# Kernel optimization log

Hardware: AMD Instinct MI355X
Metric: run time of the kernel (lower is better)

## Reference

```python
import jax, jax.numpy as jnp
import numpy as np

D_MODEL = 768
N_HEADS = 12
D_HEAD = 64
INIT_RANGE = 0.02
IGNORE = -100000.0


def setup_inputs() -> dict:
    key = jax.random.key(0)
    ks = jax.random.split(key, 5)
    x = jax.random.normal(ks[0], (2, 2048, D_MODEL), dtype=jnp.float32)
    W_Q = INIT_RANGE * jax.random.normal(ks[1], (N_HEADS, D_MODEL, D_HEAD), dtype=jnp.float32)
    W_K = INIT_RANGE * jax.random.normal(ks[2], (N_HEADS, D_MODEL, D_HEAD), dtype=jnp.float32)
    W_V = INIT_RANGE * jax.random.normal(ks[3], (N_HEADS, D_MODEL, D_HEAD), dtype=jnp.float32)
    W_O = INIT_RANGE * jax.random.normal(ks[4], (N_HEADS, D_HEAD, D_MODEL), dtype=jnp.float32)
    b_Q = jnp.zeros((N_HEADS, D_HEAD), dtype=jnp.float32)
    b_K = jnp.zeros((N_HEADS, D_HEAD), dtype=jnp.float32)
    b_V = jnp.zeros((N_HEADS, D_HEAD), dtype=jnp.float32)
    b_O = jnp.zeros((D_MODEL,), dtype=jnp.float32)
    return {"x": x, "W_Q": W_Q, "b_Q": b_Q, "W_K": W_K, "b_K": b_K,
            "W_V": W_V, "b_V": b_V, "W_O": W_O, "b_O": b_O}


def reference(x, W_Q, b_Q, W_K, b_K, W_V, b_V, W_O, b_O):
    # x: [b, s, m]; W_*: [h, m, d]
    Q = jnp.einsum('bsm,hmd->bshd', x, W_Q) + b_Q  # [b, s, h, d]
    K = jnp.einsum('bsm,hmd->bshd', x, W_K) + b_K
    V = jnp.einsum('bsm,hmd->bshd', x, W_V) + b_V
    scores = jnp.einsum('bqhd,bkhd->bhqk', Q, K) / jnp.sqrt(jnp.float32(D_HEAD))
    s = scores.shape[-1]
    causal = jnp.triu(jnp.ones((s, s), dtype=bool), k=1)  # True above diagonal
    scores = jnp.where(causal, jnp.float32(IGNORE), scores)
    pattern = jax.nn.softmax(scores, axis=-1)  # [b, h, q, k]
    Z = jnp.einsum('bhqk,bkhd->bqhd', pattern, V)
    out = jnp.einsum('bqhd,hdm->bqm', Z, W_O) + b_O
    return out
```

## Files before the change

kernel.cpp:

```cpp
#include <hip/hip_runtime.h>
#include <hip/hip_bf16.h>

#define BATCH 2
#define SLEN 2048
#define NH 12
#define DM 768
#define DH 64
#define ROWS (BATCH*SLEN)
#define NQKV (3*DM)
#define NCHUNK 40

typedef __attribute__((ext_vector_type(8))) short bf16x8;
typedef __attribute__((ext_vector_type(4))) float f32x4;
typedef __attribute__((ext_vector_type(16))) float f32x16;
typedef unsigned short u16;
typedef unsigned int u32;
typedef __attribute__((ext_vector_type(4))) unsigned short u16x4;
typedef __attribute__((ext_vector_type(8))) unsigned short u16x8;

__device__ __forceinline__ u16 f2b(float f) {
    unsigned int u = __builtin_bit_cast(unsigned int, f);
    unsigned int r = (u + 0x7FFFu + ((u >> 16) & 1u)) >> 16;
    return (u16)r;
}
__device__ __forceinline__ float b2f(u16 v) {
    unsigned int u = ((unsigned int)v) << 16;
    return __builtin_bit_cast(float, u);
}

__device__ __forceinline__ void gload16(const u16* g, u16* l) {
    __builtin_amdgcn_global_load_lds(
        (const __attribute__((address_space(1))) unsigned int*)g,
        (__attribute__((address_space(3))) unsigned int*)l,
        16, 0, 0);
}


__global__ __launch_bounds__(256) void pack_all(const float* __restrict__ x,
                                                const float* __restrict__ WQ, const float* __restrict__ WK,
                                                const float* __restrict__ WV, const float* __restrict__ WO,
                                                u16* __restrict__ xb, u16* __restrict__ wqkv,
                                                u16* __restrict__ wo) {
    __shared__ u16 L[64 * 72];
    int blk = blockIdx.x;
    int t = threadIdx.x;
    if (blk < 1536) {
        int i = blk * 256 + t;
        const float4* xv = (const float4*)x;
        float4 a = xv[i * 2], b = xv[i * 2 + 1];
        u16x8 o;
        o[0] = f2b(a.x); o[1] = f2b(a.y); o[2] = f2b(a.z); o[3] = f2b(a.w);
        o[4] = f2b(b.x); o[5] = f2b(b.y); o[6] = f2b(b.z); o[7] = f2b(b.w);
        *(u16x8*)(xb + (size_t)i * 8) = o;
    } else if (blk < 1968) {
        int idx = blk - 1536;
        int mt = idx % 12, h = (idx / 12) % 12, sel = idx / 144;
        const float* W = sel == 0 ? WQ : (sel == 1 ? WK : WV);
        const float* src = W + ((size_t)h * DM + mt * 64) * DH;
        for (int j = 0; j < 4; j++) {
            int i = t + 256 * j;
            int r = i >> 4, cf = i & 15;
            float4 v = ((const float4*)src)[i];
            u16x4 o; o[0] = f2b(v.x); o[1] = f2b(v.y); o[2] = f2b(v.z); o[3] = f2b(v.w);
            *(u16x4*)&L[r * 72 + cf * 4] = o;
        }
        __syncthreads();
        u16* orow = wqkv + ((size_t)(sel * DM + h * DH)) * DM + mt * 64;
        for (int j = 0; j < 16; j++) {
            int e = t + 256 * j;
            int d = e >> 6, mm = e & 63;
            orow[(size_t)d * DM + mm] = L[mm * 72 + d];
        }
    } else {
        int idx = blk - 1968;
        int bi = idx % 12, bj = idx / 12;
        for (int j = 0; j < 4; j++) {
            int i = t + 256 * j;
            int r = i >> 4, cf = i & 15;
            float4 v = ((const float4*)(WO + (size_t)(bi * 64 + r) * DM + bj * 64))[cf];
            u16x4 o; o[0] = f2b(v.x); o[1] = f2b(v.y); o[2] = f2b(v.z); o[3] = f2b(v.w);
            *(u16x4*)&L[r * 72 + cf * 4] = o;
        }
        __syncthreads();
        for (int j = 0; j < 16; j++) {
            int e = t + 256 * j;
            int c = e >> 6, r = e & 63;
            wo[(size_t)(bj * 64 + c) * DM + bi * 64 + r] = L[r * 72 + c];
        }
    }
}


__global__ __launch_bounds__(256) void gemm_qkv(const u16* __restrict__ A, const u16* __restrict__ Bt,
                                                const float* __restrict__ bQ, const float* __restrict__ bK,
                                                const float* __restrict__ bV,
                                                u16* __restrict__ Qb, u16* __restrict__ Kb, u16* __restrict__ Vb) {
    __shared__ u16 S[128 * 64 + 96 * 64];
    u16* Al = S;
    u16* Bl = S + 128 * 64;
    int t = threadIdx.x;
    int n0 = blockIdx.x * 96, m0 = blockIdx.y * 128;
    int lane = t & 63, w = t >> 6;
    int ln = lane & 15, qd = lane >> 4;
    int wr = (w & 1) * 64, wc = (w >> 1) * 48;
    int srow = lane >> 3, slot = lane & 7;
    f32x4 acc[4][3] = {};

    for (int kt = 0; kt < DM / 64; kt++) {
        __syncthreads();
        for (int j = 0; j < 4; j++) {
            int r = w * 32 + j * 8 + srow;
            int gc = slot ^ (r & 7);
            gload16(A + (size_t)(m0 + r) * DM + kt * 64 + gc * 8, &Al[(w * 32 + j * 8) * 64]);
        }
        for (int j = 0; j < 3; j++) {
            int r = w * 24 + j * 8 + srow;
            int gc = slot ^ (r & 7);
            gload16(Bt + (size_t)(n0 + r) * DM + kt * 64 + gc * 8, &Bl[(w * 24 + j * 8) * 64]);
        }
        __syncthreads();
        for (int ks = 0; ks < 2; ks++) {
            int sl = ((ks * 4 + qd) ^ (ln & 7)) * 8;
            bf16x8 af[4], bfr[3];
            for (int rt = 0; rt < 4; rt++)
                af[rt] = *(const bf16x8*)&Al[(wr + rt * 16 + ln) * 64 + sl];
            for (int ct = 0; ct < 3; ct++)
                bfr[ct] = *(const bf16x8*)&Bl[(wc + ct * 16 + ln) * 64 + sl];
            for (int rt = 0; rt < 4; rt++)
                for (int ct = 0; ct < 3; ct++)
                    acc[rt][ct] = __builtin_amdgcn_mfma_f32_16x16x32_bf16(af[rt], bfr[ct], acc[rt][ct], 0, 0, 0);
        }
    }
    int sel = n0 / DM;
    if (sel == 2) {
        __syncthreads();
        for (int ct = 0; ct < 3; ct++) {
            int c = wc + ct * 16 + ln;
            float bv = bV[n0 - 2 * DM + c];
            for (int rt = 0; rt < 4; rt++) {
                int s = wr + rt * 16 + qd * 4;
                for (int r = 0; r < 4; r++)
                    S[c * 136 + s + r] = f2b(acc[rt][ct][r] + bv);
            }
        }
        __syncthreads();
        int bb = m0 >> 11, ss0 = m0 & 2047;
        for (int it = 0; it < 6; it++) {
            int e = t + it * 256;
            int c = e >> 4, ck = e & 15;
            int gcol = n0 - 2 * DM + c;
            int hh = gcol >> 6, dd = gcol & 63;
            u16x8 v = *(const u16x8*)&S[c * 136 + ck * 8];
            *(u16x8*)&Vb[(((size_t)bb * NH + hh) * DH + dd) * SLEN + ss0 + ck * 8] = v;
        }
    } else {
        const float* bias = sel == 0 ? bQ : bK;
        u16* Out = sel == 0 ? Qb : Kb;
        const float qs = sel == 0 ? 0.125f * 1.44269504f : 1.0f;
        for (int ct = 0; ct < 3; ct++) {
            int col = n0 - sel * DM + wc + ct * 16 + ln;
            int hh = col >> 6, dd = col & 63;
            float bv = bias[col];
            for (int rt = 0; rt < 4; rt++) {
                int row = m0 + wr + rt * 16 + qd * 4;
                for (int r = 0; r < 4; r++) {
                    int rg = row + r;
                    int bb = rg >> 11, ss = rg & 2047;
                    Out[(((size_t)bb * NH + hh) * SLEN + ss) * DH + dd] = f2b((acc[rt][ct][r] + bv) * qs);
                }
            }
        }
    }
}


__device__ __forceinline__ void cid2qc(int cid, int& qt, int& c, int& nc) {
    if (cid < 4)       { qt = cid;                   c = 0;               nc = 1; }
    else if (cid < 12) { qt = 4 + ((cid - 4) >> 1);  c = (cid - 4) & 1;   nc = 2; }
    else if (cid < 24) { qt = 8 + (cid - 12) / 3;    c = (cid - 12) % 3;  nc = 3; }
    else               { qt = 12 + ((cid - 24) >> 2); c = (cid - 24) & 3; nc = 4; }
}

__global__ __launch_bounds__(256, 4) void attn(const u16* __restrict__ Qb, const u16* __restrict__ Kb,
                                               const u16* __restrict__ Vtg,
                                               u16* __restrict__ Po, float* __restrict__ Plv) {
    __shared__ u16 Kl[2][64 * 64];
    __shared__ u16 Vt[2][64 * 64];
    __shared__ u16 Pq[4][32 * 32];
    int blk = blockIdx.x;
    int cid = (NCHUNK - 1) - blk / 24;
    int j24 = blk % 24;
    int bh = (j24 & 7) * 3 + (j24 >> 3);
    int qt, c, nc;
    cid2qc(cid, qt, c, nc);
    int ntiles = 2 * qt + 2;
    int kt0 = c * ntiles / nc, kt1 = (c + 1) * ntiles / nc;
    const u16* Qp = Qb + (size_t)bh * SLEN * DH;
    const u16* Kp = Kb + (size_t)bh * SLEN * DH;
    const u16* Vp = Vtg + (size_t)bh * SLEN * DH;
    int t = threadIdx.x, lane = t & 63, w = t >> 6;
    int l31 = lane & 31, h = lane >> 5;
    int qg = qt * 128 + w * 32 + l31;
    int srow = lane >> 3, slot = lane & 7;
    int sw = ((l31 >> 1) & 3) << 3;

    bf16x8 qf[4];
    for (int ks = 0; ks < 4; ks++)
        qf[ks] = *(const bf16x8*)(Qp + (size_t)qg * DH + ks * 16 + h * 8);

    f32x16 o[2] = {};
    float lsum = 0.f;
    u16* Pw = Pq[w];

    auto stage = [&](int kt, int buf) {
        int k0 = kt * 64;
        for (int j = 0; j < 2; j++) {
            int r = w * 16 + j * 8 + srow;
            int gc = slot ^ (r & 7);
            gload16(Kp + (size_t)(k0 + r) * DH + gc * 8, &Kl[buf][(w * 16 + j * 8) * 64]);
            gload16(Vp + (size_t)r * SLEN + k0 + gc * 8, &Vt[buf][(w * 16 + j * 8) * 64]);
        }
    };

    stage(kt0, 0);
    __syncthreads();
    int cur = 0;
    for (int kt = kt0; kt < kt1; kt++) {
        int k0 = kt * 64;
        if (kt + 1 < kt1) stage(kt + 1, cur ^ 1);
        const u16* Kc = Kl[cur];
        const u16* Vc = Vt[cur];

        for (int kb = 0; kb < 2; kb++) {
            f32x16 sf = {};
            for (int ks = 0; ks < 4; ks++) {
                int row = kb * 32 + l31;
                bf16x8 kf = *(const bf16x8*)&Kc[row * 64 + (((ks * 2 + h) ^ (row & 7)) * 8)];
                sf = __builtin_amdgcn_mfma_f32_32x32x16_bf16(kf, qf[ks], sf, 0, 0, 0);
            }
            if (k0 + 63 > qt * 128 + w * 32) {
                for (int r = 0; r < 16; r++) {
                    int kg = k0 + kb * 32 + (r & 3) + 8 * (r >> 2) + 4 * h;
                    if (kg > qg) sf[r] = -1e30f;
                }
            }
            u32 pr[8];
            for (int p = 0; p < 8; p++) {
                u32 e0 = __builtin_bit_cast(u32, exp2f(sf[2 * p]));
                u32 e1 = __builtin_bit_cast(u32, exp2f(sf[2 * p + 1]));
                pr[p] = __builtin_amdgcn_perm(e1, e0, 0x07060302u);
            }
            for (int p = 0; p < 8; p++) {
                lsum += __builtin_bit_cast(float, pr[p] << 16);
                lsum += __builtin_bit_cast(float, pr[p] & 0xFFFF0000u);
            }
            {
                uint2 s;
                s.x = pr[0]; s.y = pr[1];
                *(uint2*)&Pw[l31 * 32 + ((4 * h) ^ sw)] = s;
                s.x = pr[2]; s.y = pr[3];
                *(uint2*)&Pw[l31 * 32 + ((8 + 4 * h) ^ sw)] = s;
                s.x = pr[4]; s.y = pr[5];
                *(uint2*)&Pw[l31 * 32 + ((16 + 4 * h) ^ sw)] = s;
                s.x = pr[6]; s.y = pr[7];
                *(uint2*)&Pw[l31 * 32 + ((24 + 4 * h) ^ sw)] = s;
            }
            for (int cc = 0; cc < 2; cc++) {
                bf16x8 pf = *(const bf16x8*)&Pw[l31 * 32 + ((cc * 16 + 8 * h) ^ sw)];
                int ch4 = kb * 2 + cc;
                for (int db = 0; db < 2; db++) {
                    int row = db * 32 + l31;
                    bf16x8 vf = *(const bf16x8*)&Vc[row * 64 + (((ch4 * 2 + h) ^ (row & 7)) * 8)];
                    o[db] = __builtin_amdgcn_mfma_f32_32x32x16_bf16(vf, pf, o[db], 0, 0, 0);
                }
            }
        }
        __syncthreads();
        cur ^= 1;
    }

    size_t pid = (size_t)bh * NCHUNK + cid;
    u16* op = Po + pid * (128 * 64);
    for (int db = 0; db < 2; db++)
        for (int rq = 0; rq < 4; rq++) {
            u16x4 ov;
            for (int j = 0; j < 4; j++) ov[j] = f2b(o[db][rq * 4 + j]);
            *(u16x4*)&op[(w * 32 + l31) * 64 + db * 32 + rq * 8 + 4 * h] = ov;
        }
    lsum += __shfl_xor(lsum, 32, 64);
    if (h == 0)
        Plv[pid * 128 + w * 32 + l31] = lsum;
}


__global__ __launch_bounds__(256) void combine(const u16* __restrict__ Po, const float* __restrict__ Plv,
                                               u16* __restrict__ Zb) {
    int qtile = blockIdx.x, bh = blockIdx.y;
    int b = bh / NH, hH = bh % NH;
    int nc = qtile < 4 ? 1 : (qtile < 8 ? 2 : (qtile < 12 ? 3 : 4));
    int base = qtile < 4 ? qtile
             : (qtile < 8 ? 4 + (qtile - 4) * 2
             : (qtile < 12 ? 12 + (qtile - 8) * 3
                           : 24 + (qtile - 12) * 4));
    int t = threadIdx.x;
    int q = t >> 1, dseg = (t & 1) * 32;

    float acc[32] = {};
    float lsum = 0.f;
    for (int cc = 0; cc < nc; cc++) {
        size_t pid = (size_t)bh * NCHUNK + base + cc;
        lsum += Plv[pid * 128 + q];
        const u16* op = Po + pid * (128 * 64) + q * 64 + dseg;
        for (int jj = 0; jj < 4; jj++) {
            u16x8 v = *(const u16x8*)(op + jj * 8);
            for (int e = 0; e < 8; e++)
                acc[jj * 8 + e] += b2f(v[e]);
        }
    }
    float inv = 1.0f / lsum;
    u16* Zp = Zb + ((size_t)b * SLEN + qtile * 128 + q) * DM + hH * DH + dseg;
    for (int jj = 0; jj < 4; jj++) {
        u16x8 ov;
        for (int e = 0; e < 8; e++) ov[e] = f2b(acc[jj * 8 + e] * inv);
        *(u16x8*)(Zp + jj * 8) = ov;
    }
}


__global__ __launch_bounds__(256) void gemm_proj(const u16* __restrict__ A, const u16* __restrict__ Bt,
                                                 const float* __restrict__ bO, float* __restrict__ out) {
    __shared__ u16 Al[64 * 64];
    __shared__ u16 Bl[96 * 64];
    int t = threadIdx.x;
    int n0 = blockIdx.x * 96, m0 = blockIdx.y * 64;
    int lane = t & 63, w = t >> 6;
    int ln = lane & 15, qd = lane >> 4;
    int wr = (w & 1) * 32, wc = (w >> 1) * 48;
    int srow = lane >> 3, slot = lane & 7;
    f32x4 acc[2][3] = {};

    for (int kt = 0; kt < DM / 64; kt++) {
        __syncthreads();
        for (int j = 0; j < 2; j++) {
            int r = w * 16 + j * 8 + srow;
            int gc = slot ^ (r & 7);
            gload16(A + (size_t)(m0 + r) * DM + kt * 64 + gc * 8, &Al[(w * 16 + j * 8) * 64]);
        }
        for (int j = 0; j < 3; j++) {
            int r = w * 24 + j * 8 + srow;
            int gc = slot ^ (r & 7);
            gload16(Bt + (size_t)(n0 + r) * DM + kt * 64 + gc * 8, &Bl[(w * 24 + j * 8) * 64]);
        }
        __syncthreads();
        for (int ks = 0; ks < 2; ks++) {
            int sl = ((ks * 4 + qd) ^ (ln & 7)) * 8;
            bf16x8 af[2], bfr[3];
            for (int rt = 0; rt < 2; rt++)
                af[rt] = *(const bf16x8*)&Al[(wr + rt * 16 + ln) * 64 + sl];
            for (int ct = 0; ct < 3; ct++)
                bfr[ct] = *(const bf16x8*)&Bl[(wc + ct * 16 + ln) * 64 + sl];
            for (int rt = 0; rt < 2; rt++)
                for (int ct = 0; ct < 3; ct++)
                    acc[rt][ct] = __builtin_amdgcn_mfma_f32_16x16x32_bf16(af[rt], bfr[ct], acc[rt][ct], 0, 0, 0);
        }
    }
    for (int ct = 0; ct < 3; ct++) {
        int col = n0 + wc + ct * 16 + ln;
        float bv = bO[col];
        for (int rt = 0; rt < 2; rt++) {
            int row = m0 + wr + rt * 16 + qd * 4;
            for (int r = 0; r < 4; r++)
                out[(size_t)(row + r) * DM + col] = acc[rt][ct][r] + bv;
        }
    }
}


extern "C" void kernel_launch(void* const* d_in, const int* in_sizes, int n_in,
                              void* d_out, int out_size, void* d_ws, size_t ws_size,
                              hipStream_t stream) {
    const float* x  = (const float*)d_in[0];
    const float* WQ = (const float*)d_in[1];
    const float* bQ = (const float*)d_in[2];
    const float* WK = (const float*)d_in[3];
    const float* bK = (const float*)d_in[4];
    const float* WV = (const float*)d_in[5];
    const float* bV = (const float*)d_in[6];
    const float* WO = (const float*)d_in[7];
    const float* bO = (const float*)d_in[8];
    float* out = (float*)d_out;

    u16* xb   = (u16*)d_ws;
    u16* wqkv = xb + (size_t)ROWS * DM;
    u16* wo   = wqkv + (size_t)NQKV * DM;
    u16* Qb   = wo + (size_t)DM * DM;
    size_t hsz = (size_t)BATCH * NH * SLEN * DH;
    u16* Kb   = Qb + hsz;
    u16* Vb   = Kb + hsz;
    u16* Zb   = Vb + hsz;
    u16* Po   = Zb + (size_t)ROWS * DM;
    float* Pl = (float*)(Po + (size_t)BATCH * NH * NCHUNK * 128 * 64);

    pack_all<<<2112, 256, 0, stream>>>(x, WQ, WK, WV, WO, xb, wqkv, wo);
    gemm_qkv<<<dim3(NQKV / 96, ROWS / 128), 256, 0, stream>>>(xb, wqkv, bQ, bK, bV, Qb, Kb, Vb);
    attn<<<dim3(NCHUNK * 24), 256, 0, stream>>>(Qb, Kb, Vb, Po, Pl);
    combine<<<dim3(SLEN / 128, BATCH * NH), 256, 0, stream>>>(Po, Pl, Zb);
    gemm_proj<<<dim3(DM / 96, ROWS / 64), 256, 0, stream>>>(Zb, wo, bO, out);
}
```

Before: 161.9 us.

## Stage Q/K epilogue through LDS for coalesced stores; write unsplit attention tiles directly

The QKV GEMM epilogue for Q and K now writes bf16 results into a shared-memory tile and then emits 16-byte coalesced rows to the head-major layout, instead of scattered 2-byte stores. In attention, query tiles that are not split across chunks normalize by the row sum and write Z directly, so the combine kernel only launches for the 12 split query tiles. This cuts uncoalesced global writes and combine traffic, at the cost of an extra barrier and LDS reuse in the GEMM epilogue.

```diff
diff --git a/kernel.cpp b/kernel.cpp
--- a/kernel.cpp
+++ b/kernel.cpp
@@ -132,8 +132,8 @@
         }
     }
     int sel = n0 / DM;
+    __syncthreads();
     if (sel == 2) {
-        __syncthreads();
         for (int ct = 0; ct < 3; ct++) {
             int c = wc + ct * 16 + ln;
             float bv = bV[n0 - 2 * DM + c];
@@ -158,17 +158,23 @@
         u16* Out = sel == 0 ? Qb : Kb;
         const float qs = sel == 0 ? 0.125f * 1.44269504f : 1.0f;
         for (int ct = 0; ct < 3; ct++) {
-            int col = n0 - sel * DM + wc + ct * 16 + ln;
-            int hh = col >> 6, dd = col & 63;
-            float bv = bias[col];
+            int c = wc + ct * 16 + ln;
+            float bv = bias[n0 - sel * DM + c];
             for (int rt = 0; rt < 4; rt++) {
-                int row = m0 + wr + rt * 16 + qd * 4;
-                for (int r = 0; r < 4; r++) {
-                    int rg = row + r;
-                    int bb = rg >> 11, ss = rg & 2047;
-                    Out[(((size_t)bb * NH + hh) * SLEN + ss) * DH + dd] = f2b((acc[rt][ct][r] + bv) * qs);
-                }
-            }
+                int s = wr + rt * 16 + qd * 4;
+                for (int r = 0; r < 4; r++)
+                    S[(s + r) * 104 + c] = f2b((acc[rt][ct][r] + bv) * qs);
+            }
+        }
+        __syncthreads();
+        int bb = m0 >> 11, ss0 = m0 & 2047;
+        for (int it = 0; it < 6; it++) {
+            int e = t + it * 256;
+            int s = e / 12, c8 = (e - s * 12) * 8;
+            int gcol = n0 - sel * DM + c8;
+            int hh = gcol >> 6, dd = gcol & 63;
+            u16x8 v = *(const u16x8*)&S[s * 104 + c8];
+            *(u16x8*)&Out[(((size_t)bb * NH + hh) * SLEN + ss0 + s) * DH + dd] = v;
         }
     }
 }
@@ -183,7 +189,8 @@
 
 __global__ __launch_bounds__(256, 4) void attn(const u16* __restrict__ Qb, const u16* __restrict__ Kb,
                                                const u16* __restrict__ Vtg,
-                                               u16* __restrict__ Po, float* __restrict__ Plv) {
+                                               u16* __restrict__ Po, float* __restrict__ Plv,
+                                               u16* __restrict__ Zb) {
     __shared__ u16 Kl[2][64 * 64];
     __shared__ u16 Vt[2][64 * 64];
     __shared__ u16 Pq[4][32 * 32];
@@ -279,29 +286,40 @@
         cur ^= 1;
     }
 
-    size_t pid = (size_t)bh * NCHUNK + cid;
-    u16* op = Po + pid * (128 * 64);
-    for (int db = 0; db < 2; db++)
-        for (int rq = 0; rq < 4; rq++) {
-            u16x4 ov;
-            for (int j = 0; j < 4; j++) ov[j] = f2b(o[db][rq * 4 + j]);
-            *(u16x4*)&op[(w * 32 + l31) * 64 + db * 32 + rq * 8 + 4 * h] = ov;
-        }
     lsum += __shfl_xor(lsum, 32, 64);
-    if (h == 0)
-        Plv[pid * 128 + w * 32 + l31] = lsum;
+    if (nc == 1) {
+        float inv = 1.0f / lsum;
+        int b = bh / NH, hH = bh % NH;
+        u16* Zp = Zb + ((size_t)b * SLEN + qg) * DM + hH * DH;
+        for (int db = 0; db < 2; db++)
+            for (int rq = 0; rq < 4; rq++) {
+                u16x4 ov;
+                for (int j = 0; j < 4; j++) ov[j] = f2b(o[db][rq * 4 + j] * inv);
+                *(u16x4*)&Zp[db * 32 + rq * 8 + 4 * h] = ov;
+            }
+    } else {
+        size_t pid = (size_t)bh * NCHUNK + cid;
+        u16* op = Po + pid * (128 * 64);
+        for (int db = 0; db < 2; db++)
+            for (int rq = 0; rq < 4; rq++) {
+                u16x4 ov;
+                for (int j = 0; j < 4; j++) ov[j] = f2b(o[db][rq * 4 + j]);
+                *(u16x4*)&op[(w * 32 + l31) * 64 + db * 32 + rq * 8 + 4 * h] = ov;
+            }
+        if (h == 0)
+            Plv[pid * 128 + w * 32 + l31] = lsum;
+    }
 }
 
 
 __global__ __launch_bounds__(256) void combine(const u16* __restrict__ Po, const float* __restrict__ Plv,
                                                u16* __restrict__ Zb) {
-    int qtile = blockIdx.x, bh = blockIdx.y;
+    int qtile = blockIdx.x + 4, bh = blockIdx.y;
     int b = bh / NH, hH = bh % NH;
-    int nc = qtile < 4 ? 1 : (qtile < 8 ? 2 : (qtile < 12 ? 3 : 4));
-    int base = qtile < 4 ? qtile
-             : (qtile < 8 ? 4 + (qtile - 4) * 2
+    int nc = qtile < 8 ? 2 : (qtile < 12 ? 3 : 4);
+    int base = qtile < 8 ? 4 + (qtile - 4) * 2
              : (qtile < 12 ? 12 + (qtile - 8) * 3
-                           : 24 + (qtile - 12) * 4));
+                           : 24 + (qtile - 12) * 4);
     int t = threadIdx.x;
     int q = t >> 1, dseg = (t & 1) * 32;
 
@@ -403,7 +421,7 @@
 
     pack_all<<<2112, 256, 0, stream>>>(x, WQ, WK, WV, WO, xb, wqkv, wo);
     gemm_qkv<<<dim3(NQKV / 96, ROWS / 128), 256, 0, stream>>>(xb, wqkv, bQ, bK, bV, Qb, Kb, Vb);
-    attn<<<dim3(NCHUNK * 24), 256, 0, stream>>>(Qb, Kb, Vb, Po, Pl);
-    combine<<<dim3(SLEN / 128, BATCH * NH), 256, 0, stream>>>(Po, Pl, Zb);
+    attn<<<dim3(NCHUNK * 24), 256, 0, stream>>>(Qb, Kb, Vb, Po, Pl, Zb);
+    combine<<<dim3(12, BATCH * NH), 256, 0, stream>>>(Po, Pl, Zb);
     gemm_proj<<<dim3(DM / 96, ROWS / 64), 256, 0, stream>>>(Zb, wo, bO, out);
 }
```

After: 160.0 us. About the same (-1.2%).
